# Kernel tuning notes

Hardware: AMD Instinct MI355X
Metric: run time of the kernel (lower is better)

Reference implementation:

```python
import jax, jax.numpy as jnp
import numpy as np

NUM_HEADS = 16
BLOCK_SIZE = 64
NUM_RANDOM_BLOCKS = 2


def _make_sparse_mask(seq_len: int) -> np.ndarray:
    # Block-diagonal pattern: token i attends to tokens in the same block.
    blk = np.arange(seq_len) // BLOCK_SIZE
    mask = blk[:, None] == blk[None, :]
    # Random extra symmetric connections (torch.randint analogue, fixed seed).
    rng = np.random.default_rng(0)
    for _ in range(NUM_RANDOM_BLOCKS):
        i = int(rng.integers(0, seq_len))
        j = int(rng.integers(0, seq_len))
        mask[i, j] = True
        mask[j, i] = True
    return mask


def setup_inputs() -> dict:
    key = jax.random.key(0)
    B, S, E = 1, 4096, 1024
    ks = jax.random.split(key, 9)
    scale = 1.0 / np.sqrt(E)
    x = jax.random.normal(ks[0], (B, S, E), dtype=jnp.float32)
    Wq = jax.random.normal(ks[1], (E, E), dtype=jnp.float32) * scale
    bq = jax.random.normal(ks[2], (E,), dtype=jnp.float32) * 0.01
    Wk = jax.random.normal(ks[3], (E, E), dtype=jnp.float32) * scale
    bk = jax.random.normal(ks[4], (E,), dtype=jnp.float32) * 0.01
    Wv = jax.random.normal(ks[5], (E, E), dtype=jnp.float32) * scale
    bv = jax.random.normal(ks[6], (E,), dtype=jnp.float32) * 0.01
    Wo = jax.random.normal(ks[7], (E, E), dtype=jnp.float32) * scale
    bo = jax.random.normal(ks[8], (E,), dtype=jnp.float32) * 0.01
    sparse_mask = jnp.asarray(_make_sparse_mask(S))
    return {"x": x, "Wq": Wq, "bq": bq, "Wk": Wk, "bk": bk,
            "Wv": Wv, "bv": bv, "Wo": Wo, "bo": bo,
            "sparse_mask": sparse_mask}


def reference(x, Wq, bq, Wk, bk, Wv, bv, Wo, bo, sparse_mask):
    B, S, E = x.shape
    H = NUM_HEADS
    D = E // H
    # Linear projections (torch Linear: y = x @ W.T + b), split into heads.
    def proj(W, b):
        y = jnp.einsum('bse,fe->bsf', x, W) + b
        return y.reshape(B, S, H, D).transpose(0, 2, 1, 3)  # [B,H,S,D]
    Q = proj(Wq, bq)
    K = proj(Wk, bk)
    V = proj(Wv, bv)
    scores = jnp.einsum('bhqd,bhkd->bhqk', Q, K) / jnp.sqrt(jnp.float32(D))
    scores = jnp.where(sparse_mask, scores, jnp.float32(-1e9))
    attn = jax.nn.softmax(scores, axis=-1)  # dropout is identity in eval
    out = jnp.einsum('bhqk,bhkd->bhqd', attn, V)
    out = out.transpose(0, 2, 1, 3).reshape(B, S, E)
    out = jnp.einsum('bse,fe->bsf', out, Wo) + bo
    return out, attn
```

## Files before the change

### kernel.cpp

```cpp
#include <hip/hip_runtime.h>
#include <cstdint>
#include <cstddef>


#define S_LEN 4096
#define EMB   1024
#define NHEAD 16
#define HDIM  64
#define NBLK  64

struct GemmPtrs {
  const float* W[3];
  const float* b[3];
  float* C[3];
};

__global__ __launch_bounds__(256) void gemm_bt_f32(const float* __restrict__ A,
                                                   GemmPtrs p, int M, int N, int K)
{
  const int z = blockIdx.z;
  const float* __restrict__ W    = p.W[z];
  const float* __restrict__ bias = p.b[z];
  float* __restrict__ C          = p.C[z];

  __shared__ float As[16][132];
  __shared__ float Bs[16][132];

  const int tid = threadIdx.x;
  const int tx = tid & 15;
  const int ty = tid >> 4;
  const int m0 = blockIdx.y * 128;
  const int n0 = blockIdx.x * 128;

  const int r0 = tid >> 2;
  const int c4 = tid & 3;

  const float* Ap  = A + (size_t)(m0 + r0) * K + c4 * 4;
  const float* Ap2 = Ap + (size_t)64 * K;
  const float* Wp  = W + (size_t)(n0 + r0) * K + c4 * 4;
  const float* Wp2 = Wp + (size_t)64 * K;

  float acc[8][8];
  #pragma unroll
  for (int i = 0; i < 8; ++i)
    #pragma unroll
    for (int j = 0; j < 8; ++j) acc[i][j] = 0.f;

  for (int k0 = 0; k0 < K; k0 += 16) {
    const float4 a0 = *(const float4*)(Ap  + k0);
    const float4 a1 = *(const float4*)(Ap2 + k0);
    const float4 w0 = *(const float4*)(Wp  + k0);
    const float4 w1 = *(const float4*)(Wp2 + k0);
    __syncthreads();
    As[c4*4+0][r0]    = a0.x; As[c4*4+1][r0]    = a0.y;
    As[c4*4+2][r0]    = a0.z; As[c4*4+3][r0]    = a0.w;
    As[c4*4+0][64+r0] = a1.x; As[c4*4+1][64+r0] = a1.y;
    As[c4*4+2][64+r0] = a1.z; As[c4*4+3][64+r0] = a1.w;
    Bs[c4*4+0][r0]    = w0.x; Bs[c4*4+1][r0]    = w0.y;
    Bs[c4*4+2][r0]    = w0.z; Bs[c4*4+3][r0]    = w0.w;
    Bs[c4*4+0][64+r0] = w1.x; Bs[c4*4+1][64+r0] = w1.y;
    Bs[c4*4+2][64+r0] = w1.z; Bs[c4*4+3][64+r0] = w1.w;
    __syncthreads();

    #pragma unroll
    for (int k = 0; k < 16; ++k) {
      const float4 av0 = *(const float4*)&As[k][ty*4];
      const float4 av1 = *(const float4*)&As[k][64 + ty*4];
      const float4 bv0 = *(const float4*)&Bs[k][tx*4];
      const float4 bv1 = *(const float4*)&Bs[k][64 + tx*4];
      const float av[8] = {av0.x, av0.y, av0.z, av0.w, av1.x, av1.y, av1.z, av1.w};
      const float bv[8] = {bv0.x, bv0.y, bv0.z, bv0.w, bv1.x, bv1.y, bv1.z, bv1.w};
      #pragma unroll
      for (int i = 0; i < 8; ++i)
        #pragma unroll
        for (int j = 0; j < 8; ++j)
          acc[i][j] += av[i] * bv[j];
    }
  }

  #pragma unroll
  for (int i = 0; i < 8; ++i) {
    const int row = m0 + (i >> 2) * 64 + ty * 4 + (i & 3);
    #pragma unroll
    for (int jg = 0; jg < 2; ++jg) {
      const int col = n0 + jg * 64 + tx * 4;
      const float4 bb = *(const float4*)&bias[col];
      float4 o;
      o.x = acc[i][jg*4+0] + bb.x;
      o.y = acc[i][jg*4+1] + bb.y;
      o.z = acc[i][jg*4+2] + bb.z;
      o.w = acc[i][jg*4+3] + bb.w;
      *(float4*)&C[(size_t)row * N + col] = o;
    }
  }
}

__global__ void probe_mode(const unsigned char* __restrict__ mask,
                           int* __restrict__ flags)
{
  if (blockIdx.x == 0 && threadIdx.x == 0) {
    int lsb = 0, msb3f = 0;
    #pragma unroll
    for (int t = 0; t < 8; ++t) {
      lsb   += (mask[64 + 4 * t] != 0) ? 1 : 0;
      msb3f += (mask[4 * t + 3] == 0x3f) ? 1 : 0;
    }
    flags[0] = (lsb >= 4 || msb3f >= 4) ? 1 : 0;
  }
}

__global__ void scan_mask(const unsigned char* __restrict__ mask,
                          const int* __restrict__ flags,
                          int* __restrict__ cnt, int* __restrict__ pairs)
{
  const int stride = gridDim.x * blockDim.x;
  const int t0 = blockIdx.x * blockDim.x + threadIdx.x;
  if (flags[0] == 0) {
    const uint4* m4 = (const uint4*)mask;
    const int n4 = (S_LEN * S_LEN) / 16;
    for (int i = t0; i < n4; i += stride) {
      const uint4 v = m4[i];
      if ((v.x | v.y | v.z | v.w) != 0u) {
        const unsigned int wv[4] = {v.x, v.y, v.z, v.w};
        #pragma unroll
        for (int wi = 0; wi < 4; ++wi)
          #pragma unroll
          for (int bi = 0; bi < 4; ++bi)
            if ((wv[wi] >> (8 * bi)) & 0xffu) {
              const int idx = i * 16 + wi * 4 + bi;
              const int r = idx >> 12, c = idx & 4095;
              if ((r >> 6) != (c >> 6)) {
                const int s = atomicAdd(cnt, 1);
                if (s < 64) pairs[s] = (r << 12) | c;
              }
            }
      }
    }
  } else {
    const uint4* m4 = (const uint4*)mask;
    const int n4 = (S_LEN * S_LEN) / 4;
    for (int i = t0; i < n4; i += stride) {
      const uint4 v = m4[i];
      if ((v.x | v.y | v.z | v.w) != 0u) {
        const unsigned int wv[4] = {v.x, v.y, v.z, v.w};
        #pragma unroll
        for (int wi = 0; wi < 4; ++wi)
          if (wv[wi] != 0u) {
            const int idx = i * 4 + wi;
            const int r = idx >> 12, c = idx & 4095;
            if ((r >> 6) != (c >> 6)) {
              const int s = atomicAdd(cnt, 1);
              if (s < 64) pairs[s] = (r << 12) | c;
            }
          }
      }
    }
  }
}

__global__ __launch_bounds__(256) void sparse_attn(
    const float* __restrict__ Qg, const float* __restrict__ Kg,
    const float* __restrict__ Vg, float* __restrict__ ctx,
    float* __restrict__ attn, const int* __restrict__ cntp,
    const int* __restrict__ pairs)
{
  __shared__ float Qs[64][64];
  __shared__ float Ks[64][68];
  __shared__ float Vs[64][64];
  __shared__ float P[64][64];
  __shared__ float exP[64][8];
  __shared__ int   exK[64][8];
  __shared__ int   exCnt[64];

  const int qb  = blockIdx.x;
  const int h   = blockIdx.y;
  const int s0  = qb * 64;
  const int tid = threadIdx.x;

  for (int f = tid; f < 64 * 16; f += 256) {
    const int r  = f >> 4;
    const int cc = (f & 15) * 4;
    const size_t g = (size_t)(s0 + r) * EMB + h * HDIM + cc;
    const float4 q4 = *(const float4*)(Qg + g);
    const float4 k4 = *(const float4*)(Kg + g);
    const float4 v4 = *(const float4*)(Vg + g);
    *(float4*)&Qs[r][cc] = q4;
    *(float4*)&Ks[r][cc] = k4;
    *(float4*)&Vs[r][cc] = v4;
  }
  __syncthreads();

  const int lane = tid & 63;
  const int wq   = tid >> 6;

  float kreg[64];
  #pragma unroll
  for (int d4 = 0; d4 < 16; ++d4) {
    const float4 kv = *(const float4*)&Ks[lane][d4 * 4];
    kreg[d4*4+0] = kv.x; kreg[d4*4+1] = kv.y;
    kreg[d4*4+2] = kv.z; kreg[d4*4+3] = kv.w;
  }

  #pragma unroll
  for (int it = 0; it < 16; ++it) {
    const int q = it * 4 + wq;
    float acc = 0.f;
    #pragma unroll
    for (int d4 = 0; d4 < 16; ++d4) {
      const float4 qv = *(const float4*)&Qs[q][d4 * 4];
      acc += qv.x * kreg[d4*4+0] + qv.y * kreg[d4*4+1]
           + qv.z * kreg[d4*4+2] + qv.w * kreg[d4*4+3];
    }
    const int sw = q & 15;
    P[q][(((lane >> 2) ^ sw) << 2) + (lane & 3)] = acc * 0.125f;
  }
  __syncthreads();

  if (tid < 64) {
    const int q   = tid;
    const int sw  = q & 15;
    const int row = s0 + q;
    float m = -1e30f;
    #pragma unroll
    for (int j = 0; j < 64; ++j) {
      const int pos = (((j >> 2) ^ sw) << 2) + (j & 3);
      m = fmaxf(m, P[q][pos]);
    }
    int ec = 0;
    int np = *cntp; if (np > 64) np = 64;
    for (int t = 0; t < np; ++t) {
      const int pr = pairs[t];
      if ((pr >> 12) == row) {
        const int pj = pr & 4095;
        const float* kp = Kg + (size_t)pj * EMB + h * HDIM;
        float s = 0.f;
        for (int d = 0; d < 64; ++d) s += Qs[q][d] * kp[d];
        s *= 0.125f;
        if (ec < 8) { exK[q][ec] = pj; exP[q][ec] = s; ++ec; }
      }
    }
    for (int e = 0; e < ec; ++e) m = fmaxf(m, exP[q][e]);
    float sum = 0.f;
    #pragma unroll
    for (int j = 0; j < 64; ++j) {
      const int pos = (((j >> 2) ^ sw) << 2) + (j & 3);
      const float v = expf(P[q][pos] - m);
      P[q][pos] = v;
      sum += v;
    }
    for (int e = 0; e < ec; ++e) { const float v = expf(exP[q][e] - m); exP[q][e] = v; sum += v; }
    const float inv = 1.0f / sum;
    #pragma unroll
    for (int j = 0; j < 64; ++j) {
      const int pos = (((j >> 2) ^ sw) << 2) + (j & 3);
      P[q][pos] *= inv;
    }
    for (int e = 0; e < ec; ++e) {
      const float pv = exP[q][e] * inv;
      exP[q][e] = pv;
      attn[((size_t)h * S_LEN + row) * S_LEN + exK[q][e]] = pv;
    }
    exCnt[q] = ec;
  }
  __syncthreads();

  float vcol[64];
  #pragma unroll
  for (int k = 0; k < 64; ++k) vcol[k] = Vs[k][lane];

  #pragma unroll
  for (int it = 0; it < 16; ++it) {
    const int q  = it * 4 + wq;
    const int sw = q & 15;
    float acc = 0.f;
    #pragma unroll
    for (int k4 = 0; k4 < 16; ++k4) {
      const float4 pv = *(const float4*)&P[q][(k4 ^ sw) << 2];
      acc += pv.x * vcol[k4*4+0] + pv.y * vcol[k4*4+1]
           + pv.z * vcol[k4*4+2] + pv.w * vcol[k4*4+3];
    }
    const int ec = exCnt[q];
    for (int e = 0; e < ec; ++e)
      acc += exP[q][e] * Vg[(size_t)exK[q][e] * EMB + h * HDIM + lane];
    ctx[(size_t)(s0 + q) * EMB + h * HDIM + lane] = acc;
  }

  for (int f = tid; f < 4096; f += 256) {
    const int q  = f >> 6;
    const int k  = f & 63;
    const int sw = q & 15;
    const int pos = (((k >> 2) ^ sw) << 2) + (k & 3);
    attn[((size_t)h * S_LEN + s0 + q) * S_LEN + s0 + k] = P[q][pos];
  }
}

extern "C" void kernel_launch(void* const* d_in, const int* in_sizes, int n_in,
                              void* d_out, int out_size, void* d_ws, size_t ws_size,
                              hipStream_t stream)
{
  (void)in_sizes; (void)n_in; (void)out_size; (void)ws_size;

  const float* x  = (const float*)d_in[0];
  const float* Wq = (const float*)d_in[1];
  const float* bq = (const float*)d_in[2];
  const float* Wk = (const float*)d_in[3];
  const float* bk = (const float*)d_in[4];
  const float* Wv = (const float*)d_in[5];
  const float* bv = (const float*)d_in[6];
  const float* Wo = (const float*)d_in[7];
  const float* bo = (const float*)d_in[8];
  const unsigned char* mask = (const unsigned char*)d_in[9];

  float* out  = (float*)d_out;
  float* attn = out + (size_t)S_LEN * EMB;

  float* Q    = (float*)d_ws;
  float* ctx  = Q;
  float* Kb   = Q   + (size_t)S_LEN * EMB;
  float* Vb   = Kb  + (size_t)S_LEN * EMB;
  int*   flags = (int*)(Vb + (size_t)S_LEN * EMB);
  int*   cnt   = flags + 1;
  int*   pairs = flags + 2;

  hipMemsetAsync(attn, 0, (size_t)NHEAD * S_LEN * S_LEN * sizeof(float), stream);
  hipMemsetAsync(flags, 0, (2 + 64) * sizeof(int), stream);

  probe_mode<<<1, 1, 0, stream>>>(mask, flags);
  scan_mask<<<2048, 256, 0, stream>>>(mask, flags, cnt, pairs);

  GemmPtrs pq;
  pq.W[0] = Wq; pq.W[1] = Wk; pq.W[2] = Wv;
  pq.b[0] = bq; pq.b[1] = bk; pq.b[2] = bv;
  pq.C[0] = Q;  pq.C[1] = Kb; pq.C[2] = Vb;
  gemm_bt_f32<<<dim3(EMB / 128, S_LEN / 128, 3), 256, 0, stream>>>(x, pq, S_LEN, EMB, EMB);

  sparse_attn<<<dim3(NBLK, NHEAD), 256, 0, stream>>>(Q, Kb, Vb, ctx, attn, cnt, pairs);

  GemmPtrs po;
  po.W[0] = Wo; po.W[1] = Wo; po.W[2] = Wo;
  po.b[0] = bo; po.b[1] = bo; po.b[2] = bo;
  po.C[0] = out; po.C[1] = out; po.C[2] = out;
  gemm_bt_f32<<<dim3(EMB / 128, S_LEN / 128, 1), 256, 0, stream>>>(ctx, po, S_LEN, EMB, EMB);
}
```

Before: 1.562 ms.

## Use split-bf16 MFMA GEMMs for projections and replace memset with fill kernel

Adds a three-term bf16 hi/lo split GEMM on MFMA instructions that approximates fp32 accuracy, replacing the scalar fp32 SIMT GEMMs for the Q/K/V and output projections when enough workspace is available. Inputs and weights are split into hi/lo bf16 planes by separate kernels before each GEMM. The attention-matrix memset is also replaced by a custom vectorized zero-fill kernel. The aim is to move the projection work onto matrix cores, at the cost of extra split passes, more kernel launches and a small loss of precision.

```diff
diff --git a/kernel.cpp b/kernel.cpp
--- a/kernel.cpp
+++ b/kernel.cpp
@@ -9,6 +9,138 @@
 #define HDIM  64
 #define NBLK  64
 
+typedef short bf16x8 __attribute__((ext_vector_type(8)));
+typedef float f32x4  __attribute__((ext_vector_type(4)));
+
+__global__ __launch_bounds__(256) void zero_fill(uint4* __restrict__ p, size_t n)
+{
+  size_t i = (size_t)blockIdx.x * blockDim.x + threadIdx.x;
+  const size_t stride = (size_t)gridDim.x * blockDim.x;
+  const uint4 z = {0u, 0u, 0u, 0u};
+  for (; i < n; i += stride) p[i] = z;
+}
+
+__device__ __forceinline__ void split1(float v, unsigned short& h, unsigned short& l)
+{
+  const unsigned b  = __float_as_uint(v);
+  const unsigned hr = (b + 0x8000u) >> 16;
+  h = (unsigned short)hr;
+  const float rem = v - __uint_as_float(hr << 16);
+  l = (unsigned short)((__float_as_uint(rem) + 0x8000u) >> 16);
+}
+
+__global__ __launch_bounds__(256) void split_f32_bf16(
+    const float* __restrict__ in, unsigned short* __restrict__ hi,
+    unsigned short* __restrict__ lo, int n4)
+{
+  int i = blockIdx.x * blockDim.x + threadIdx.x;
+  const int stride = gridDim.x * blockDim.x;
+  for (; i < n4; i += stride) {
+    const float4 v = ((const float4*)in)[i];
+    ushort4 h, l;
+    split1(v.x, h.x, l.x);
+    split1(v.y, h.y, l.y);
+    split1(v.z, h.z, l.z);
+    split1(v.w, h.w, l.w);
+    ((ushort4*)hi)[i] = h;
+    ((ushort4*)lo)[i] = l;
+  }
+}
+
+__global__ __launch_bounds__(256) void gemm_mfma_split(
+    const unsigned short* __restrict__ Ahi, const unsigned short* __restrict__ Alo,
+    const unsigned short* __restrict__ Bhi, const unsigned short* __restrict__ Blo,
+    const float* __restrict__ bias, float* __restrict__ C, int M, int N, int K)
+{
+  __shared__ unsigned short sAh[128 * 40];
+  __shared__ unsigned short sAl[128 * 40];
+  __shared__ unsigned short sBh[128 * 40];
+  __shared__ unsigned short sBl[128 * 40];
+
+  const int tid  = threadIdx.x;
+  const int m0   = blockIdx.y * 128;
+  const int n0   = blockIdx.x * 128;
+  const int lane = tid & 63;
+  const int wave = tid >> 6;
+  const int wr   = wave >> 1;
+  const int wc   = wave & 1;
+  const int r16  = lane & 15;
+  const int kc   = lane >> 4;
+
+  const int rt = tid >> 1;
+  const int ht = tid & 1;
+  const unsigned short* gAh = Ahi + (size_t)(m0 + rt) * K + ht * 16;
+  const unsigned short* gAl = Alo + (size_t)(m0 + rt) * K + ht * 16;
+  const unsigned short* gBh = Bhi + (size_t)(n0 + rt) * K + ht * 16;
+  const unsigned short* gBl = Blo + (size_t)(n0 + rt) * K + ht * 16;
+  const int lds_off = rt * 40 + ht * 16;
+
+  f32x4 acc[4][4];
+  #pragma unroll
+  for (int i = 0; i < 4; ++i)
+    #pragma unroll
+    for (int j = 0; j < 4; ++j) acc[i][j] = (f32x4){0.f, 0.f, 0.f, 0.f};
+
+  for (int k0 = 0; k0 < K; k0 += 32) {
+    const uint4 vah0 = *(const uint4*)(gAh + k0);
+    const uint4 vah1 = *(const uint4*)(gAh + k0 + 8);
+    const uint4 val0 = *(const uint4*)(gAl + k0);
+    const uint4 val1 = *(const uint4*)(gAl + k0 + 8);
+    const uint4 vbh0 = *(const uint4*)(gBh + k0);
+    const uint4 vbh1 = *(const uint4*)(gBh + k0 + 8);
+    const uint4 vbl0 = *(const uint4*)(gBl + k0);
+    const uint4 vbl1 = *(const uint4*)(gBl + k0 + 8);
+
+    __syncthreads();
+    *(uint4*)&sAh[lds_off]     = vah0;
+    *(uint4*)&sAh[lds_off + 8] = vah1;
+    *(uint4*)&sAl[lds_off]     = val0;
+    *(uint4*)&sAl[lds_off + 8] = val1;
+    *(uint4*)&sBh[lds_off]     = vbh0;
+    *(uint4*)&sBh[lds_off + 8] = vbh1;
+    *(uint4*)&sBl[lds_off]     = vbl0;
+    *(uint4*)&sBl[lds_off + 8] = vbl1;
+    __syncthreads();
+
+    bf16x8 ah[4], al[4], bh[4], bl[4];
+    #pragma unroll
+    for (int mf = 0; mf < 4; ++mf) {
+      const int row = wr * 64 + mf * 16 + r16;
+      ah[mf] = *(const bf16x8*)&sAh[row * 40 + kc * 8];
+      al[mf] = *(const bf16x8*)&sAl[row * 40 + kc * 8];
+    }
+    #pragma unroll
+    for (int nf = 0; nf < 4; ++nf) {
+      const int col = wc * 64 + nf * 16 + r16;
+      bh[nf] = *(const bf16x8*)&sBh[col * 40 + kc * 8];
+      bl[nf] = *(const bf16x8*)&sBl[col * 40 + kc * 8];
+    }
+    #pragma unroll
+    for (int mf = 0; mf < 4; ++mf)
+      #pragma unroll
+      for (int nf = 0; nf < 4; ++nf) {
+        acc[mf][nf] = __builtin_amdgcn_mfma_f32_16x16x32_bf16(ah[mf], bh[nf], acc[mf][nf], 0, 0, 0);
+        acc[mf][nf] = __builtin_amdgcn_mfma_f32_16x16x32_bf16(ah[mf], bl[nf], acc[mf][nf], 0, 0, 0);
+        acc[mf][nf] = __builtin_amdgcn_mfma_f32_16x16x32_bf16(al[mf], bh[nf], acc[mf][nf], 0, 0, 0);
+      }
+  }
+
+  const int fq = lane >> 4;
+  #pragma unroll
+  for (int mf = 0; mf < 4; ++mf) {
+    #pragma unroll
+    for (int nf = 0; nf < 4; ++nf) {
+      const int col = n0 + wc * 64 + nf * 16 + r16;
+      const float bb = bias[col];
+      #pragma unroll
+      for (int v = 0; v < 4; ++v) {
+        const int row = m0 + wr * 64 + mf * 16 + fq * 4 + v;
+        C[(size_t)row * N + col] = acc[mf][nf][v] + bb;
+      }
+    }
+  }
+}
+
 struct GemmPtrs {
   const float* W[3];
   const float* b[3];
@@ -31,7 +163,6 @@
   const int ty = tid >> 4;
   const int m0 = blockIdx.y * 128;
   const int n0 = blockIdx.x * 128;
-
   const int r0 = tid >> 2;
   const int c4 = tid & 3;
 
@@ -298,7 +429,7 @@
                               void* d_out, int out_size, void* d_ws, size_t ws_size,
                               hipStream_t stream)
 {
-  (void)in_sizes; (void)n_in; (void)out_size; (void)ws_size;
+  (void)in_sizes; (void)n_in; (void)out_size;
 
   const float* x  = (const float*)d_in[0];
   const float* Wq = (const float*)d_in[1];
@@ -314,31 +445,58 @@
   float* out  = (float*)d_out;
   float* attn = out + (size_t)S_LEN * EMB;
 
-  float* Q    = (float*)d_ws;
-  float* ctx  = Q;
-  float* Kb   = Q   + (size_t)S_LEN * EMB;
-  float* Vb   = Kb  + (size_t)S_LEN * EMB;
-  int*   flags = (int*)(Vb + (size_t)S_LEN * EMB);
-  int*   cnt   = flags + 1;
-  int*   pairs = flags + 2;
-
-  hipMemsetAsync(attn, 0, (size_t)NHEAD * S_LEN * S_LEN * sizeof(float), stream);
+  char* ws = (char*)d_ws;
+  const size_t MB = 1024 * 1024;
+  float* Q   = (float*)(ws + 0 * MB);
+  float* ctx = Q;
+  float* Kb  = (float*)(ws + 16 * MB);
+  float* Vb  = (float*)(ws + 32 * MB);
+
+  const bool use_mfma = (ws_size >= 69 * MB);
+
+  unsigned short* Ahi = (unsigned short*)(ws + 48 * MB);
+  unsigned short* Alo = (unsigned short*)(ws + 56 * MB);
+  unsigned short* Whi = (unsigned short*)(ws + 64 * MB);
+  unsigned short* Wlo = (unsigned short*)(ws + 66 * MB);
+  int* flags = (int*)(ws + (use_mfma ? 68 * MB : 48 * MB));
+  int* cnt   = flags + 1;
+  int* pairs = flags + 2;
+
+  zero_fill<<<2048, 256, 0, stream>>>((uint4*)attn,
+                                      (size_t)NHEAD * S_LEN * S_LEN / 4);
   hipMemsetAsync(flags, 0, (2 + 64) * sizeof(int), stream);
 
   probe_mode<<<1, 1, 0, stream>>>(mask, flags);
   scan_mask<<<2048, 256, 0, stream>>>(mask, flags, cnt, pairs);
 
-  GemmPtrs pq;
-  pq.W[0] = Wq; pq.W[1] = Wk; pq.W[2] = Wv;
-  pq.b[0] = bq; pq.b[1] = bk; pq.b[2] = bv;
-  pq.C[0] = Q;  pq.C[1] = Kb; pq.C[2] = Vb;
-  gemm_bt_f32<<<dim3(EMB / 128, S_LEN / 128, 3), 256, 0, stream>>>(x, pq, S_LEN, EMB, EMB);
-
-  sparse_attn<<<dim3(NBLK, NHEAD), 256, 0, stream>>>(Q, Kb, Vb, ctx, attn, cnt, pairs);
-
-  GemmPtrs po;
-  po.W[0] = Wo; po.W[1] = Wo; po.W[2] = Wo;
-  po.b[0] = bo; po.b[1] = bo; po.b[2] = bo;
-  po.C[0] = out; po.C[1] = out; po.C[2] = out;
-  gemm_bt_f32<<<dim3(EMB / 128, S_LEN / 128, 1), 256, 0, stream>>>(ctx, po, S_LEN, EMB, EMB);
-}
+  if (use_mfma) {
+    const dim3 ggrid(EMB / 128, S_LEN / 128);
+    split_f32_bf16<<<1024, 256, 0, stream>>>(x, Ahi, Alo, S_LEN * EMB / 4);
+    split_f32_bf16<<<512, 256, 0, stream>>>(Wq, Whi, Wlo, EMB * EMB / 4);
+    gemm_mfma_split<<<ggrid, 256, 0, stream>>>(Ahi, Alo, Whi, Wlo, bq, Q,  S_LEN, EMB, EMB);
+    split_f32_bf16<<<512, 256, 0, stream>>>(Wk, Whi, Wlo, EMB * EMB / 4);
+    gemm_mfma_split<<<ggrid, 256, 0, stream>>>(Ahi, Alo, Whi, Wlo, bk, Kb, S_LEN, EMB, EMB);
+    split_f32_bf16<<<512, 256, 0, stream>>>(Wv, Whi, Wlo, EMB * EMB / 4);
+    gemm_mfma_split<<<ggrid, 256, 0, stream>>>(Ahi, Alo, Whi, Wlo, bv, Vb, S_LEN, EMB, EMB);
+
+    sparse_attn<<<dim3(NBLK, NHEAD), 256, 0, stream>>>(Q, Kb, Vb, ctx, attn, cnt, pairs);
+
+    split_f32_bf16<<<1024, 256, 0, stream>>>(ctx, Ahi, Alo, S_LEN * EMB / 4);
+    split_f32_bf16<<<512, 256, 0, stream>>>(Wo, Whi, Wlo, EMB * EMB / 4);
+    gemm_mfma_split<<<ggrid, 256, 0, stream>>>(Ahi, Alo, Whi, Wlo, bo, out, S_LEN, EMB, EMB);
+  } else {
+    GemmPtrs pq;
+    pq.W[0] = Wq; pq.W[1] = Wk; pq.W[2] = Wv;
+    pq.b[0] = bq; pq.b[1] = bk; pq.b[2] = bv;
+    pq.C[0] = Q;  pq.C[1] = Kb; pq.C[2] = Vb;
+    gemm_bt_f32<<<dim3(EMB / 128, S_LEN / 128, 3), 256, 0, stream>>>(x, pq, S_LEN, EMB, EMB);
+
+    sparse_attn<<<dim3(NBLK, NHEAD), 256, 0, stream>>>(Q, Kb, Vb, ctx, attn, cnt, pairs);
+
+    GemmPtrs po;
+    po.W[0] = Wo; po.W[1] = Wo; po.W[2] = Wo;
+    po.b[0] = bo; po.b[1] = bo; po.b[2] = bo;
+    po.C[0] = out; po.C[1] = out; po.C[2] = out;
+    gemm_bt_f32<<<dim3(EMB / 128, S_LEN / 128, 1), 256, 0, stream>>>(ctx, po, S_LEN, EMB, EMB);
+  }
+}
```

Result: faster. 1.436 ms (-8.0%).
